# Kernel optimization log

Hardware: AMD Instinct MI355X
Metric: run time of the kernel (lower is better)

## Reference

```python
import jax, jax.numpy as jnp
import numpy as np

T = 5            # Newton-Schulz iterations
NORM_GROUPS = 16 # groups along out_channels
EPS = 1e-5


def setup_inputs() -> dict:
    key = jax.random.key(0)
    # conv weight: [out_ch, in_ch, kh, kw]
    weight = jax.random.normal(key, (2048, 1024, 3, 3), dtype=jnp.float32) * 0.05
    return {"weight": weight}


def reference(weight):
    g = NORM_GROUPS
    out_ch = weight.shape[0]
    Z = weight.reshape(g, out_ch // g, -1)                 # [g, n, d]
    Zc = Z - Z.mean(axis=-1, keepdims=True)                # center each row
    S = jnp.einsum('gnd,gmd->gnm', Zc, Zc)                 # [g, n, n] covariance
    n = S.shape[-1]
    eye = jnp.eye(n, dtype=S.dtype)
    S = S + EPS * eye
    norm_S = jnp.sqrt(jnp.sum(S * S, axis=(1, 2), keepdims=True))  # fro norm, [g,1,1]
    S = S / norm_S

    B0 = jnp.broadcast_to(eye, S.shape)                    # B[0] = I

    def body(B, _):
        B3 = B @ B @ B                                     # matrix_power3
        Bn = 1.5 * B - 0.5 * (B3 @ S)                      # baddbmm(1.5, B, -0.5, B^3, S)
        return Bn, None

    Bt, _ = jax.lax.scan(body, B0, None, length=T)
    W = (Bt @ Zc) / jnp.sqrt(norm_S)                       # [g, n, d]
    return W.reshape(weight.shape)
```

## Files before the change

### kernel.cpp

```cpp
#include <hip/hip_runtime.h>


#define G 16
#define NROW 128
#define D 9216
#define OC 2048
#define KSPLIT 16
#define KCHUNK 576
#define EPSV 1e-5f

typedef float f32x16 __attribute__((ext_vector_type(16)));
typedef __bf16 bf16x8 __attribute__((ext_vector_type(8)));

union Frag {
    uint4 q;
    unsigned short s[8];
    bf16x8 v;
};

static __device__ __forceinline__ unsigned short f2bf(float x) {
    union { float f; unsigned int u; } a; a.f = x;
    unsigned int u = a.u;
    unsigned int r = u + 0x7FFFu + ((u >> 16) & 1u);
    return (unsigned short)(r >> 16);
}

static __device__ __forceinline__ float bf2f(unsigned short s) {
    union { unsigned int u; float f; } a; a.u = ((unsigned int)s) << 16;
    return a.f;
}

static __device__ __forceinline__ void lgkm_barrier() {
    asm volatile("s_waitcnt lgkmcnt(0)" ::: "memory");
    __builtin_amdgcn_s_barrier();
    __builtin_amdgcn_sched_barrier(0);
}

static __device__ __forceinline__ int swz(int r, int c) {
    return (r << 7) + ((((c >> 3) ^ (r & 15)) << 3) | (c & 7));
}

__global__ __launch_bounds__(256) void k_sgemm(const float* __restrict__ W,
                                               unsigned short* __restrict__ Zraw,
                                               float* __restrict__ Spart,
                                               float* __restrict__ rowsumPart) {
    __shared__ unsigned short tile[NROW * 128];
    __shared__ float rsum[NROW];
    int bid = blockIdx.x;
    int g = bid >> 4, ks = bid & 15;
    int t = threadIdx.x, lane = t & 63, wave = t >> 6;
    int mq = (wave & 1) * 64, nq = (wave >> 1) * 64;
    int m = lane & 31, h = lane >> 5;

    if (t < 128) rsum[t] = 0.f;

    f32x16 acc[2][2];
#pragma unroll
    for (int i = 0; i < 2; i++)
#pragma unroll
        for (int j = 0; j < 2; j++)
#pragma unroll
            for (int z = 0; z < 16; z++) acc[i][j][z] = 0.f;

    float rs[16], rsh[8];
#pragma unroll
    for (int i = 0; i < 16; i++) rs[i] = 0.f;
#pragma unroll
    for (int i = 0; i < 8; i++) rsh[i] = 0.f;

    const float* wg = W + (size_t)g * NROW * D + ks * KCHUNK;
    unsigned short* zo = Zraw + (size_t)g * NROW * D + ks * KCHUNK;

    float4 pf[16];
#pragma unroll
    for (int p = 0; p < 16; p++) {
        int fl = p * 256 + t, r = fl >> 5, cf = fl & 31;
        pf[p] = *(const float4*)(wg + (size_t)r * D + cf * 4);
    }

    for (int step = 0; step < 5; step++) {
        lgkm_barrier();
        if (step < 4) {
            int dbase = step * 128;
#pragma unroll
            for (int p = 0; p < 16; p++) {
                int fl = p * 256 + t, r = fl >> 5, cf = fl & 31;
                float4 x = pf[p];
                rs[p] += x.x + x.y + x.z + x.w;
                ushort4 pk;
                pk.x = f2bf(x.x); pk.y = f2bf(x.y);
                pk.z = f2bf(x.z); pk.w = f2bf(x.w);
                *(ushort4*)(zo + (size_t)r * D + dbase + cf * 4) = pk;
                union { ushort4 s4; uint2 u; } cv; cv.s4 = pk;
                *(uint2*)(tile + swz(r, cf * 4)) = cv.u;
            }
        } else {
#pragma unroll
            for (int p = 0; p < 8; p++) {
                int fl = p * 256 + t, r = fl >> 4, cf = fl & 15;
                float4 x = pf[p];
                rsh[p] += x.x + x.y + x.z + x.w;
                ushort4 pk;
                pk.x = f2bf(x.x); pk.y = f2bf(x.y);
                pk.z = f2bf(x.z); pk.w = f2bf(x.w);
                *(ushort4*)(zo + (size_t)r * D + 512 + cf * 4) = pk;
                union { ushort4 s4; uint2 u; } cv; cv.s4 = pk;
                *(uint2*)(tile + swz(r, cf * 4)) = cv.u;
            }
        }
        lgkm_barrier();
        if (step < 3) {
            int dbase = (step + 1) * 128;
#pragma unroll
            for (int p = 0; p < 16; p++) {
                int fl = p * 256 + t, r = fl >> 5, cf = fl & 31;
                pf[p] = *(const float4*)(wg + (size_t)r * D + dbase + cf * 4);
            }
        } else if (step == 3) {
#pragma unroll
            for (int p = 0; p < 8; p++) {
                int fl = p * 256 + t, r = fl >> 4, cf = fl & 15;
                pf[p] = *(const float4*)(wg + (size_t)r * D + 512 + cf * 4);
            }
        }
        int kmax = (step < 4) ? 8 : 4;
#pragma unroll
        for (int kk = 0; kk < 8; kk++) {
            if (kk >= kmax) break;
            int kb = kk * 16 + h * 8;
            Frag a0, a1, b0, b1;
            a0.q = *(const uint4*)(tile + swz(mq + m, kb));
            a1.q = *(const uint4*)(tile + swz(mq + 32 + m, kb));
            b0.q = *(const uint4*)(tile + swz(nq + m, kb));
            b1.q = *(const uint4*)(tile + swz(nq + 32 + m, kb));
            acc[0][0] = __builtin_amdgcn_mfma_f32_32x32x16_bf16(a0.v, b0.v, acc[0][0], 0, 0, 0);
            acc[0][1] = __builtin_amdgcn_mfma_f32_32x32x16_bf16(a0.v, b1.v, acc[0][1], 0, 0, 0);
            acc[1][0] = __builtin_amdgcn_mfma_f32_32x32x16_bf16(a1.v, b0.v, acc[1][0], 0, 0, 0);
            acc[1][1] = __builtin_amdgcn_mfma_f32_32x32x16_bf16(a1.v, b1.v, acc[1][1], 0, 0, 0);
        }
    }
    float* sp = Spart + (size_t)bid * 16384;
#pragma unroll
    for (int i = 0; i < 2; i++)
#pragma unroll
        for (int j = 0; j < 2; j++)
#pragma unroll
            for (int reg = 0; reg < 16; reg++) {
                int row = (reg & 3) + 8 * (reg >> 2) + 4 * h;
                sp[(mq + i * 32 + row) * 128 + nq + j * 32 + m] = acc[i][j][reg];
            }
#pragma unroll
    for (int p = 0; p < 16; p++) atomicAdd(&rsum[p * 8 + (t >> 5)], rs[p]);
#pragma unroll
    for (int p = 0; p < 8; p++) atomicAdd(&rsum[p * 16 + (t >> 4)], rsh[p]);
    lgkm_barrier();
    if (t < 128) rowsumPart[bid * 128 + t] = rsum[t];
}

__global__ __launch_bounds__(256) void k_reduce(const float* __restrict__ Spart,
                                                const float* __restrict__ rowsumPart,
                                                float* __restrict__ Sred,
                                                float* __restrict__ normPart) {
    __shared__ float muv[128];
    __shared__ float ls[4];
    int b = blockIdx.x;
    int g = b >> 4, part = b & 15;
    int t = threadIdx.x;
    if (t < 128) {
        float s = 0.f;
        for (int ks = 0; ks < KSPLIT; ks++) s += rowsumPart[(g * 16 + ks) * 128 + t];
        muv[t] = s * (1.0f / 9216.0f);
    }
    __syncthreads();
    int el = part * 1024 + t * 4;
    float4 s = {0.f, 0.f, 0.f, 0.f};
    for (int ks = 0; ks < KSPLIT; ks++) {
        float4 p = *(const float4*)(Spart + (size_t)(g * KSPLIT + ks) * 16384 + el);
        s.x += p.x; s.y += p.y; s.z += p.z; s.w += p.w;
    }
    int r = el >> 7, c = el & 127;
    float4 mc = *(float4*)&muv[c];
    float dm = 9216.0f * muv[r];
    s.x -= dm * mc.x; s.y -= dm * mc.y; s.z -= dm * mc.z; s.w -= dm * mc.w;
    if (r >= c && r <= c + 3) {
        if (r == c) s.x += EPSV;
        else if (r == c + 1) s.y += EPSV;
        else if (r == c + 2) s.z += EPSV;
        else s.w += EPSV;
    }
    *(float4*)(Sred + (size_t)g * 16384 + el) = s;
    float sq = s.x * s.x + s.y * s.y + s.z * s.z + s.w * s.w;
#pragma unroll
    for (int o = 32; o > 0; o >>= 1) sq += __shfl_down(sq, o, 64);
    if ((t & 63) == 0) ls[t >> 6] = sq;
    __syncthreads();
    if (t == 0) normPart[b] = ls[0] + ls[1] + ls[2] + ls[3];
}

__global__ __launch_bounds__(512) void k_ns(const float* __restrict__ Sred,
                                            const float* __restrict__ normPart,
                                            const float* __restrict__ rowsumPart,
                                            unsigned short* __restrict__ Bt,
                                            float* __restrict__ cvec) {
    extern __shared__ unsigned short sm[];
    unsigned short* Bb = sm;
    unsigned short* Sb = sm + 16384;
    unsigned short* Ub = sm + 32768;
    unsigned short* Vt = sm + 49152;
    int g = blockIdx.x;
    int t = threadIdx.x, lane = t & 63, wave = t >> 6;
    int m = lane & 31, h = lane >> 5;

    float ns = 0.f;
#pragma unroll
    for (int i = 0; i < 16; i++) ns += normPart[g * 16 + i];
    float rn = 1.0f / sqrtf(ns);

    {
        int r = t >> 2, c0 = (t & 3) * 32;
        const float* sp = Sred + (size_t)g * 16384 + r * 128 + c0;
#pragma unroll
        for (int q = 0; q < 4; q++) {
            int c = c0 + q * 8;
            float4 x0 = *(const float4*)(sp + q * 8);
            float4 x1 = *(const float4*)(sp + q * 8 + 4);
            float vv[8] = {x0.x, x0.y, x0.z, x0.w, x1.x, x1.y, x1.z, x1.w};
            Frag fs, fb;
#pragma unroll
            for (int i = 0; i < 8; i++) {
                float sv = vv[i] * rn;
                fs.s[i] = f2bf(sv);
                float bv = -0.5f * sv + ((r == c + i) ? 1.5f : 0.f);
                fb.s[i] = f2bf(bv);
            }
            *(uint4*)(Sb + swz(r, c)) = fs.q;
            *(uint4*)(Bb + swz(r, c)) = fb.q;
        }
    }
    Frag fI[2];
#pragma unroll
    for (int kk2 = 0; kk2 < 2; kk2++)
#pragma unroll
        for (int j = 0; j < 8; j++)
            fI[kk2].s[j] = (m == kk2 * 16 + h * 8 + j) ? (unsigned short)0x3FC0
                                                       : (unsigned short)0;
    __syncthreads();

    for (int iter = 0; iter < 4; iter++) {
#pragma unroll
        for (int i = 0; i < 4; i++) {
            int task = wave * 4 + i;
            int tmb = ((task >> 2) & 3) * 32, tnb = (task & 3) * 32;
            const unsigned short* Bsrc = (task < 16) ? Bb : Sb;
            unsigned short* dst = (task < 16) ? Ub : Vt;
            float sc = (task < 16) ? 1.0f : -0.5f;
            f32x16 acc;
#pragma unroll
            for (int z = 0; z < 16; z++) acc[z] = 0.f;
#pragma unroll
            for (int kk = 0; kk < 8; kk++) {
                Frag a, bfr;
                a.q = *(const uint4*)(Bb + swz(tmb + m, kk * 16 + h * 8));
                bfr.q = *(const uint4*)(Bsrc + swz(tnb + m, kk * 16 + h * 8));
                acc = __builtin_amdgcn_mfma_f32_32x32x16_bf16(a.v, bfr.v, acc, 0, 0, 0);
            }
#pragma unroll
            for (int q = 0; q < 4; q++) {
                union { unsigned short s[4]; uint2 u; } pk;
#pragma unroll
                for (int j = 0; j < 4; j++) pk.s[j] = f2bf(sc * acc[q * 4 + j]);
                *(uint2*)(dst + swz(tnb + m, tmb + q * 8 + h * 4)) = pk.u;
            }
        }
        __syncthreads();
        f32x16 acc2[2];
#pragma unroll
        for (int i = 0; i < 2; i++) {
            int task = wave * 2 + i;
            int tmb = (task >> 2) * 32, tnb = (task & 3) * 32;
#pragma unroll
            for (int z = 0; z < 16; z++) acc2[i][z] = 0.f;
#pragma unroll
            for (int kk = 0; kk < 8; kk++) {
                Frag a, bfr;
                a.q = *(const uint4*)(Ub + swz(tmb + m, kk * 16 + h * 8));
                bfr.q = *(const uint4*)(Vt + swz(tnb + m, kk * 16 + h * 8));
                acc2[i] = __builtin_amdgcn_mfma_f32_32x32x16_bf16(a.v, bfr.v, acc2[i], 0, 0, 0);
            }
#pragma unroll
            for (int kk2 = 0; kk2 < 2; kk2++) {
                Frag bfr;
                bfr.q = *(const uint4*)(Bb + swz(tnb + m, tmb + kk2 * 16 + h * 8));
                acc2[i] = __builtin_amdgcn_mfma_f32_32x32x16_bf16(fI[kk2].v, bfr.v, acc2[i], 0, 0, 0);
            }
        }
        __syncthreads();
#pragma unroll
        for (int i = 0; i < 2; i++) {
            int task = wave * 2 + i;
            int tmb = (task >> 2) * 32, tnb = (task & 3) * 32;
#pragma unroll
            for (int q = 0; q < 4; q++) {
                union { unsigned short s[4]; uint2 u; } pk;
#pragma unroll
                for (int j = 0; j < 4; j++) pk.s[j] = f2bf(acc2[i][q * 4 + j]);
                *(uint2*)(Bb + swz(tnb + m, tmb + q * 8 + h * 4)) = pk.u;
            }
        }
        __syncthreads();
    }
    {
        int r = t >> 2, c0 = (t & 3) * 32;
        unsigned short* bp = Bt + (size_t)g * 16384 + r * 128;
#pragma unroll
        for (int q = 0; q < 4; q++) {
            uint4 dd = *(const uint4*)(Bb + swz(r, c0 + q * 8));
            *(uint4*)(bp + c0 + q * 8) = dd;
        }
    }
    float* muv = (float*)(sm + 32768);
    if (t < 128) {
        float s = 0.f;
        for (int ks = 0; ks < KSPLIT; ks++) s += rowsumPart[(g * 16 + ks) * 128 + t];
        muv[t] = s * (1.0f / 9216.0f);
    }
    __syncthreads();
    if (t < 128) {
        float cacc = 0.f;
        for (int k = 0; k < 128; k++) cacc += bf2f(Bb[swz(t, k)]) * muv[k];
        cvec[g * 128 + t] = cacc;
    }
}

__global__ __launch_bounds__(256) void k_wgemm(const unsigned short* __restrict__ Zraw,
                                               const unsigned short* __restrict__ Bt,
                                               const float* __restrict__ normPart,
                                               const float* __restrict__ cvec,
                                               float* __restrict__ out) {
    __shared__ unsigned short Ab[16384];
    __shared__ unsigned short Zt[16384];
    __shared__ float cs[128];
    int nt = blockIdx.x, g = blockIdx.y;
    int t = threadIdx.x, lane = t & 63, wave = t >> 6;
    int m = lane & 31, h = lane >> 5;

    float nsum = 0.f;
#pragma unroll
    for (int i = 0; i < 16; i++) nsum += normPart[g * 16 + i];
    float ss = 1.0f / sqrtf(sqrtf(nsum));

    const unsigned short* bg = Bt + (size_t)g * 16384;
    const unsigned short* zg = Zraw + (size_t)g * NROW * D + nt * 128;
#pragma unroll
    for (int p = 0; p < 8; p++) {
        int flat = p * 256 + t;
        int r = flat >> 4, gc = flat & 15;
        uint4 da = *(const uint4*)(bg + r * 128 + gc * 8);
        uint4 dz = *(const uint4*)(zg + (size_t)r * D + gc * 8);
        *(uint4*)(Ab + swz(r, gc * 8)) = da;
        *(uint4*)(Zt + swz(r, gc * 8)) = dz;
    }
    if (t < 128) cs[t] = cvec[g * 128 + t] * ss;
    __syncthreads();

    int cw = wave * 32 + m;

    f32x16 acc[4];
#pragma unroll
    for (int i = 0; i < 4; i++)
#pragma unroll
        for (int z = 0; z < 16; z++) acc[i][z] = 0.f;

#pragma unroll
    for (int ks = 0; ks < 8; ks++) {
        int k0 = ks * 16 + h * 8;
        Frag b;
#pragma unroll
        for (int j = 0; j < 8; j++) b.s[j] = Zt[swz(k0 + j, cw)];
#pragma unroll
        for (int i = 0; i < 4; i++) {
            Frag a;
            a.q = *(const uint4*)(Ab + swz(i * 32 + m, k0));
            acc[i] = __builtin_amdgcn_mfma_f32_32x32x16_bf16(a.v, b.v, acc[i], 0, 0, 0);
        }
    }
    float* og = out + (size_t)(g * NROW) * D + nt * 128 + cw;
#pragma unroll
    for (int i = 0; i < 4; i++)
#pragma unroll
        for (int reg = 0; reg < 16; reg++) {
            int row = i * 32 + (reg & 3) + 8 * (reg >> 2) + 4 * h;
            og[(size_t)row * D] = acc[i][reg] * ss - cs[row];
        }
}

extern "C" void kernel_launch(void* const* d_in, const int* in_sizes, int n_in,
                              void* d_out, int out_size, void* d_ws, size_t ws_size,
                              hipStream_t stream) {
    const float* W = (const float*)d_in[0];
    float* out = (float*)d_out;
    char* ws = (char*)d_ws;

    unsigned short* Zraw = (unsigned short*)(ws);
    float* Spart = (float*)(ws + 37748736ULL);
    float* Sred = (float*)(ws + 54525952ULL);
    float* normPart = (float*)(ws + 55574528ULL);
    unsigned short* Bt = (unsigned short*)(ws + 55575552ULL);
    float* rowsumPart = (float*)(ws + 56099840ULL);
    float* cvec = (float*)(ws + 56230912ULL);

    k_sgemm<<<G * KSPLIT, 256, 0, stream>>>(W, Zraw, Spart, rowsumPart);
    k_reduce<<<256, 256, 0, stream>>>(Spart, rowsumPart, Sred, normPart);
    hipFuncSetAttribute((const void*)k_ns,
                        hipFuncAttributeMaxDynamicSharedMemorySize, 131072);
    k_ns<<<G, 512, 131072, stream>>>(Sred, normPart, rowsumPart, Bt, cvec);
    k_wgemm<<<dim3(72, G), 256, 0, stream>>>(Zraw, Bt, normPart, cvec, out);
}
```

Before: 185.3 us.

## Fuse four stages into one cooperative kernel with grid-wide syncs

Replaces the four separate launches (S GEMM, reduction, Newton-Schulz, output GEMM) with one cooperative kernel of 256 blocks that uses grid.sync between stages. The goal is to remove launch gaps and inter-kernel idle time. In exchange, the Newton-Schulz stage now runs with 256 threads per block instead of 512. The output GEMM is also spread over a persistent grid of 256 blocks, which reduces parallelism in those stages. If the cooperative launch fails, it falls back to the old four-kernel path.

```diff
diff --git a/kernel.cpp b/kernel.cpp
--- a/kernel.cpp
+++ b/kernel.cpp
@@ -1,5 +1,8 @@
 #include <hip/hip_runtime.h>
-
+#include <hip/hip_cooperative_groups.h>
+
+
+namespace cg = cooperative_groups;
 
 #define G 16
 #define NROW 128
@@ -38,6 +41,363 @@
 
 static __device__ __forceinline__ int swz(int r, int c) {
     return (r << 7) + ((((c >> 3) ^ (r & 15)) << 3) | (c & 7));
+}
+
+__global__ __launch_bounds__(256) void k_fused(const float* __restrict__ W,
+                                               unsigned short* __restrict__ Zraw,
+                                               float* __restrict__ Spart,
+                                               float* __restrict__ rowsumPart,
+                                               float* __restrict__ Sred,
+                                               float* __restrict__ normPart,
+                                               unsigned short* __restrict__ Bt,
+                                               float* __restrict__ cvec,
+                                               float* __restrict__ out) {
+    extern __shared__ char smraw[];
+    cg::grid_group grid = cg::this_grid();
+    int bid = blockIdx.x;
+    int t = threadIdx.x, lane = t & 63, wave = t >> 6;
+    int m = lane & 31, h = lane >> 5;
+
+    {
+        unsigned short* tile = (unsigned short*)smraw;
+        float* rsum = (float*)(smraw + 32768);
+        int g = bid >> 4, ks = bid & 15;
+        int mq = (wave & 1) * 64, nq = (wave >> 1) * 64;
+
+        if (t < 128) rsum[t] = 0.f;
+
+        f32x16 acc[2][2];
+#pragma unroll
+        for (int i = 0; i < 2; i++)
+#pragma unroll
+            for (int j = 0; j < 2; j++)
+#pragma unroll
+                for (int z = 0; z < 16; z++) acc[i][j][z] = 0.f;
+
+        float rs[16], rsh[8];
+#pragma unroll
+        for (int i = 0; i < 16; i++) rs[i] = 0.f;
+#pragma unroll
+        for (int i = 0; i < 8; i++) rsh[i] = 0.f;
+
+        const float* wg = W + (size_t)g * NROW * D + ks * KCHUNK;
+        unsigned short* zo = Zraw + (size_t)g * NROW * D + ks * KCHUNK;
+
+        float4 pf[16];
+#pragma unroll
+        for (int p = 0; p < 16; p++) {
+            int fl = p * 256 + t, r = fl >> 5, cf = fl & 31;
+            pf[p] = *(const float4*)(wg + (size_t)r * D + cf * 4);
+        }
+
+        for (int step = 0; step < 5; step++) {
+            lgkm_barrier();
+            if (step < 4) {
+                int dbase = step * 128;
+#pragma unroll
+                for (int p = 0; p < 16; p++) {
+                    int fl = p * 256 + t, r = fl >> 5, cf = fl & 31;
+                    float4 x = pf[p];
+                    rs[p] += x.x + x.y + x.z + x.w;
+                    ushort4 pk;
+                    pk.x = f2bf(x.x); pk.y = f2bf(x.y);
+                    pk.z = f2bf(x.z); pk.w = f2bf(x.w);
+                    *(ushort4*)(zo + (size_t)r * D + dbase + cf * 4) = pk;
+                    union { ushort4 s4; uint2 u; } cv; cv.s4 = pk;
+                    *(uint2*)(tile + swz(r, cf * 4)) = cv.u;
+                }
+            } else {
+#pragma unroll
+                for (int p = 0; p < 8; p++) {
+                    int fl = p * 256 + t, r = fl >> 4, cf = fl & 15;
+                    float4 x = pf[p];
+                    rsh[p] += x.x + x.y + x.z + x.w;
+                    ushort4 pk;
+                    pk.x = f2bf(x.x); pk.y = f2bf(x.y);
+                    pk.z = f2bf(x.z); pk.w = f2bf(x.w);
+                    *(ushort4*)(zo + (size_t)r * D + 512 + cf * 4) = pk;
+                    union { ushort4 s4; uint2 u; } cv; cv.s4 = pk;
+                    *(uint2*)(tile + swz(r, cf * 4)) = cv.u;
+                }
+            }
+            lgkm_barrier();
+            if (step < 3) {
+                int dbase = (step + 1) * 128;
+#pragma unroll
+                for (int p = 0; p < 16; p++) {
+                    int fl = p * 256 + t, r = fl >> 5, cf = fl & 31;
+                    pf[p] = *(const float4*)(wg + (size_t)r * D + dbase + cf * 4);
+                }
+            } else if (step == 3) {
+#pragma unroll
+                for (int p = 0; p < 8; p++) {
+                    int fl = p * 256 + t, r = fl >> 4, cf = fl & 15;
+                    pf[p] = *(const float4*)(wg + (size_t)r * D + 512 + cf * 4);
+                }
+            }
+            int kmax = (step < 4) ? 8 : 4;
+#pragma unroll
+            for (int kk = 0; kk < 8; kk++) {
+                if (kk >= kmax) break;
+                int kb = kk * 16 + h * 8;
+                Frag a0, a1, b0, b1;
+                a0.q = *(const uint4*)(tile + swz(mq + m, kb));
+                a1.q = *(const uint4*)(tile + swz(mq + 32 + m, kb));
+                b0.q = *(const uint4*)(tile + swz(nq + m, kb));
+                b1.q = *(const uint4*)(tile + swz(nq + 32 + m, kb));
+                acc[0][0] = __builtin_amdgcn_mfma_f32_32x32x16_bf16(a0.v, b0.v, acc[0][0], 0, 0, 0);
+                acc[0][1] = __builtin_amdgcn_mfma_f32_32x32x16_bf16(a0.v, b1.v, acc[0][1], 0, 0, 0);
+                acc[1][0] = __builtin_amdgcn_mfma_f32_32x32x16_bf16(a1.v, b0.v, acc[1][0], 0, 0, 0);
+                acc[1][1] = __builtin_amdgcn_mfma_f32_32x32x16_bf16(a1.v, b1.v, acc[1][1], 0, 0, 0);
+            }
+        }
+        float* sp = Spart + (size_t)bid * 16384;
+#pragma unroll
+        for (int i = 0; i < 2; i++)
+#pragma unroll
+            for (int j = 0; j < 2; j++)
+#pragma unroll
+                for (int reg = 0; reg < 16; reg++) {
+                    int row = (reg & 3) + 8 * (reg >> 2) + 4 * h;
+                    sp[(mq + i * 32 + row) * 128 + nq + j * 32 + m] = acc[i][j][reg];
+                }
+#pragma unroll
+        for (int p = 0; p < 16; p++) atomicAdd(&rsum[p * 8 + (t >> 5)], rs[p]);
+#pragma unroll
+        for (int p = 0; p < 8; p++) atomicAdd(&rsum[p * 16 + (t >> 4)], rsh[p]);
+        lgkm_barrier();
+        if (t < 128) rowsumPart[bid * 128 + t] = rsum[t];
+    }
+    __threadfence();
+    grid.sync();
+    __threadfence();
+
+    {
+        float* muv = (float*)smraw;
+        float* ls = muv + 128;
+        int g = bid >> 4, part = bid & 15;
+        if (t < 128) {
+            float s = 0.f;
+            for (int ks = 0; ks < KSPLIT; ks++) s += rowsumPart[(g * 16 + ks) * 128 + t];
+            muv[t] = s * (1.0f / 9216.0f);
+        }
+        __syncthreads();
+        int el = part * 1024 + t * 4;
+        float4 s = {0.f, 0.f, 0.f, 0.f};
+        for (int ks = 0; ks < KSPLIT; ks++) {
+            float4 p = *(const float4*)(Spart + (size_t)(g * KSPLIT + ks) * 16384 + el);
+            s.x += p.x; s.y += p.y; s.z += p.z; s.w += p.w;
+        }
+        int r = el >> 7, c = el & 127;
+        float4 mc = *(float4*)&muv[c];
+        float dm = 9216.0f * muv[r];
+        s.x -= dm * mc.x; s.y -= dm * mc.y; s.z -= dm * mc.z; s.w -= dm * mc.w;
+        if (r >= c && r <= c + 3) {
+            if (r == c) s.x += EPSV;
+            else if (r == c + 1) s.y += EPSV;
+            else if (r == c + 2) s.z += EPSV;
+            else s.w += EPSV;
+        }
+        *(float4*)(Sred + (size_t)g * 16384 + el) = s;
+        float sq = s.x * s.x + s.y * s.y + s.z * s.z + s.w * s.w;
+#pragma unroll
+        for (int o = 32; o > 0; o >>= 1) sq += __shfl_down(sq, o, 64);
+        if ((t & 63) == 0) ls[t >> 6] = sq;
+        __syncthreads();
+        if (t == 0) normPart[bid] = ls[0] + ls[1] + ls[2] + ls[3];
+    }
+    __threadfence();
+    grid.sync();
+    __threadfence();
+
+    if (bid < G) {
+        unsigned short* Bb = (unsigned short*)smraw;
+        unsigned short* Sb = Bb + 16384;
+        unsigned short* Ub = Bb + 32768;
+        unsigned short* Vt = Bb + 49152;
+        int g = bid;
+
+        float ns = 0.f;
+#pragma unroll
+        for (int i = 0; i < 16; i++) ns += normPart[g * 16 + i];
+        float rn = 1.0f / sqrtf(ns);
+
+        {
+            int r = t >> 1, c0 = (t & 1) * 64;
+            const float* sp = Sred + (size_t)g * 16384 + r * 128 + c0;
+#pragma unroll
+            for (int q = 0; q < 8; q++) {
+                int c = c0 + q * 8;
+                float4 x0 = *(const float4*)(sp + q * 8);
+                float4 x1 = *(const float4*)(sp + q * 8 + 4);
+                float vv[8] = {x0.x, x0.y, x0.z, x0.w, x1.x, x1.y, x1.z, x1.w};
+                Frag fs, fb;
+#pragma unroll
+                for (int i = 0; i < 8; i++) {
+                    float sv = vv[i] * rn;
+                    fs.s[i] = f2bf(sv);
+                    float bv = -0.5f * sv + ((r == c + i) ? 1.5f : 0.f);
+                    fb.s[i] = f2bf(bv);
+                }
+                *(uint4*)(Sb + swz(r, c)) = fs.q;
+                *(uint4*)(Bb + swz(r, c)) = fb.q;
+            }
+        }
+        Frag fI[2];
+#pragma unroll
+        for (int kk2 = 0; kk2 < 2; kk2++)
+#pragma unroll
+            for (int j = 0; j < 8; j++)
+                fI[kk2].s[j] = (m == kk2 * 16 + h * 8 + j) ? (unsigned short)0x3FC0
+                                                           : (unsigned short)0;
+        __syncthreads();
+
+        for (int iter = 0; iter < 4; iter++) {
+#pragma unroll
+            for (int i = 0; i < 8; i++) {
+                int task = wave * 8 + i;
+                int tmb = ((task >> 2) & 3) * 32, tnb = (task & 3) * 32;
+                const unsigned short* Bsrc = (task < 16) ? Bb : Sb;
+                unsigned short* dst = (task < 16) ? Ub : Vt;
+                float sc = (task < 16) ? 1.0f : -0.5f;
+                f32x16 acc;
+#pragma unroll
+                for (int z = 0; z < 16; z++) acc[z] = 0.f;
+#pragma unroll
+                for (int kk = 0; kk < 8; kk++) {
+                    Frag a, bfr;
+                    a.q = *(const uint4*)(Bb + swz(tmb + m, kk * 16 + h * 8));
+                    bfr.q = *(const uint4*)(Bsrc + swz(tnb + m, kk * 16 + h * 8));
+                    acc = __builtin_amdgcn_mfma_f32_32x32x16_bf16(a.v, bfr.v, acc, 0, 0, 0);
+                }
+#pragma unroll
+                for (int q = 0; q < 4; q++) {
+                    union { unsigned short s[4]; uint2 u; } pk;
+#pragma unroll
+                    for (int j = 0; j < 4; j++) pk.s[j] = f2bf(sc * acc[q * 4 + j]);
+                    *(uint2*)(dst + swz(tnb + m, tmb + q * 8 + h * 4)) = pk.u;
+                }
+            }
+            __syncthreads();
+            f32x16 acc2[4];
+#pragma unroll
+            for (int i = 0; i < 4; i++) {
+                int task = wave * 4 + i;
+                int tmb = (task >> 2) * 32, tnb = (task & 3) * 32;
+#pragma unroll
+                for (int z = 0; z < 16; z++) acc2[i][z] = 0.f;
+#pragma unroll
+                for (int kk = 0; kk < 8; kk++) {
+                    Frag a, bfr;
+                    a.q = *(const uint4*)(Ub + swz(tmb + m, kk * 16 + h * 8));
+                    bfr.q = *(const uint4*)(Vt + swz(tnb + m, kk * 16 + h * 8));
+                    acc2[i] = __builtin_amdgcn_mfma_f32_32x32x16_bf16(a.v, bfr.v, acc2[i], 0, 0, 0);
+                }
+#pragma unroll
+                for (int kk2 = 0; kk2 < 2; kk2++) {
+                    Frag bfr;
+                    bfr.q = *(const uint4*)(Bb + swz(tnb + m, tmb + kk2 * 16 + h * 8));
+                    acc2[i] = __builtin_amdgcn_mfma_f32_32x32x16_bf16(fI[kk2].v, bfr.v, acc2[i], 0, 0, 0);
+                }
+            }
+            __syncthreads();
+#pragma unroll
+            for (int i = 0; i < 4; i++) {
+                int task = wave * 4 + i;
+                int tmb = (task >> 2) * 32, tnb = (task & 3) * 32;
+#pragma unroll
+                for (int q = 0; q < 4; q++) {
+                    union { unsigned short s[4]; uint2 u; } pk;
+#pragma unroll
+                    for (int j = 0; j < 4; j++) pk.s[j] = f2bf(acc2[i][q * 4 + j]);
+                    *(uint2*)(Bb + swz(tnb + m, tmb + q * 8 + h * 4)) = pk.u;
+                }
+            }
+            __syncthreads();
+        }
+        {
+            int r = t >> 1, c0 = (t & 1) * 64;
+            unsigned short* bp = Bt + (size_t)g * 16384 + r * 128;
+#pragma unroll
+            for (int q = 0; q < 8; q++) {
+                uint4 dd = *(const uint4*)(Bb + swz(r, c0 + q * 8));
+                *(uint4*)(bp + c0 + q * 8) = dd;
+            }
+        }
+        float* muv = (float*)(smraw + 65536);
+        if (t < 128) {
+            float s = 0.f;
+            for (int ks = 0; ks < KSPLIT; ks++) s += rowsumPart[(g * 16 + ks) * 128 + t];
+            muv[t] = s * (1.0f / 9216.0f);
+        }
+        __syncthreads();
+        if (t < 128) {
+            float cacc = 0.f;
+            for (int k = 0; k < 128; k++) cacc += bf2f(Bb[swz(t, k)]) * muv[k];
+            cvec[g * 128 + t] = cacc;
+        }
+    }
+    __threadfence();
+    grid.sync();
+    __threadfence();
+
+    {
+        unsigned short* Ab = (unsigned short*)smraw;
+        unsigned short* Zt = Ab + 16384;
+        float* cs = (float*)(smraw + 65536);
+        for (int tilei = bid; tilei < 72 * G; tilei += 256) {
+            int nt = tilei % 72, g = tilei / 72;
+            __syncthreads();
+
+            float nsum = 0.f;
+#pragma unroll
+            for (int i = 0; i < 16; i++) nsum += normPart[g * 16 + i];
+            float ss = 1.0f / sqrtf(sqrtf(nsum));
+
+            const unsigned short* bg = Bt + (size_t)g * 16384;
+            const unsigned short* zg = Zraw + (size_t)g * NROW * D + nt * 128;
+#pragma unroll
+            for (int p = 0; p < 8; p++) {
+                int flat = p * 256 + t;
+                int r = flat >> 4, gc = flat & 15;
+                uint4 da = *(const uint4*)(bg + r * 128 + gc * 8);
+                uint4 dz = *(const uint4*)(zg + (size_t)r * D + gc * 8);
+                *(uint4*)(Ab + swz(r, gc * 8)) = da;
+                *(uint4*)(Zt + swz(r, gc * 8)) = dz;
+            }
+            if (t < 128) cs[t] = cvec[g * 128 + t] * ss;
+            __syncthreads();
+
+            int cw = wave * 32 + m;
+            f32x16 acc[4];
+#pragma unroll
+            for (int i = 0; i < 4; i++)
+#pragma unroll
+                for (int z = 0; z < 16; z++) acc[i][z] = 0.f;
+
+#pragma unroll
+            for (int ks = 0; ks < 8; ks++) {
+                int k0 = ks * 16 + h * 8;
+                Frag b;
+#pragma unroll
+                for (int j = 0; j < 8; j++) b.s[j] = Zt[swz(k0 + j, cw)];
+#pragma unroll
+                for (int i = 0; i < 4; i++) {
+                    Frag a;
+                    a.q = *(const uint4*)(Ab + swz(i * 32 + m, k0));
+                    acc[i] = __builtin_amdgcn_mfma_f32_32x32x16_bf16(a.v, b.v, acc[i], 0, 0, 0);
+                }
+            }
+            float* og = out + (size_t)(g * NROW) * D + nt * 128 + cw;
+#pragma unroll
+            for (int i = 0; i < 4; i++)
+#pragma unroll
+                for (int reg = 0; reg < 16; reg++) {
+                    int row = i * 32 + (reg & 3) + 8 * (reg >> 2) + 4 * h;
+                    og[(size_t)row * D] = acc[i][reg] * ss - cs[row];
+                }
+        }
+    }
 }
 
 __global__ __launch_bounds__(256) void k_sgemm(const float* __restrict__ W,
@@ -409,10 +769,19 @@
     float* rowsumPart = (float*)(ws + 56099840ULL);
     float* cvec = (float*)(ws + 56230912ULL);
 
-    k_sgemm<<<G * KSPLIT, 256, 0, stream>>>(W, Zraw, Spart, rowsumPart);
-    k_reduce<<<256, 256, 0, stream>>>(Spart, rowsumPart, Sred, normPart);
-    hipFuncSetAttribute((const void*)k_ns,
+    hipFuncSetAttribute((const void*)k_fused,
                         hipFuncAttributeMaxDynamicSharedMemorySize, 131072);
-    k_ns<<<G, 512, 131072, stream>>>(Sred, normPart, rowsumPart, Bt, cvec);
-    k_wgemm<<<dim3(72, G), 256, 0, stream>>>(Zraw, Bt, normPart, cvec, out);
-}
+    void* args[] = {(void*)&W, (void*)&Zraw, (void*)&Spart, (void*)&rowsumPart,
+                    (void*)&Sred, (void*)&normPart, (void*)&Bt, (void*)&cvec,
+                    (void*)&out};
+    hipError_t err = hipLaunchCooperativeKernel((const void*)k_fused, dim3(256),
+                                                dim3(256), args, 131072, stream);
+    if (err != hipSuccess) {
+        k_sgemm<<<G * KSPLIT, 256, 0, stream>>>(W, Zraw, Spart, rowsumPart);
+        k_reduce<<<256, 256, 0, stream>>>(Spart, rowsumPart, Sred, normPart);
+        hipFuncSetAttribute((const void*)k_ns,
+                            hipFuncAttributeMaxDynamicSharedMemorySize, 131072);
+        k_ns<<<G, 512, 131072, stream>>>(Sred, normPart, rowsumPart, Bt, cvec);
+        k_wgemm<<<dim3(72, G), 256, 0, stream>>>(Zraw, Bt, normPart, cvec, out);
+    }
+}
```

Result: slower. 378.2 us (+104.2%).
